# Kernel optimization log

Hardware: AMD Instinct MI355X
Metric: run time of the kernel (lower is better)

The kernel has to match this reference:

```python
import jax, jax.numpy as jnp
import numpy as np

B, S, H, NH = 4, 1024, 1024, 16
D = H // NH  # head dim = 64
MAXPOS = 1024
EPS = 1e-12


def setup_inputs() -> dict:
    key = jax.random.key(0)
    ks = jax.random.split(key, 12)
    sc = 0.02
    return {
        "hidden_states": jax.random.normal(ks[0], (B, S, H), jnp.float32),
        "attention_mask": jnp.zeros((B, 1, 1, S), jnp.float32),
        "Wq": jax.random.normal(ks[1], (H, H), jnp.float32) * sc,
        "bq": jnp.zeros((H,), jnp.float32),
        "Wk": jax.random.normal(ks[2], (H, H), jnp.float32) * sc,
        "bk": jnp.zeros((H,), jnp.float32),
        "Wv": jax.random.normal(ks[3], (H, H), jnp.float32) * sc,
        "bv": jnp.zeros((H,), jnp.float32),
        "dist_emb": jax.random.normal(ks[4], (2 * MAXPOS - 1, D), jnp.float32) * sc,
        "Wo": jax.random.normal(ks[5], (H, H), jnp.float32) * sc,
        "bo": jnp.zeros((H,), jnp.float32),
        "ln_g": jnp.ones((H,), jnp.float32),
        "ln_b": jnp.zeros((H,), jnp.float32),
    }


def _heads(x):  # [B,S,H] -> [B,NH,S,D]
    return x.reshape(B, S, NH, D).transpose(0, 2, 1, 3)


def reference(hidden_states, attention_mask, Wq, bq, Wk, bk, Wv, bv,
              dist_emb, Wo, bo, ln_g, ln_b):
    x = hidden_states
    q = _heads(x @ Wq.T + bq)  # [B,NH,S,D]
    k = _heads(x @ Wk.T + bk)
    v = _heads(x @ Wv.T + bv)

    scores = jnp.einsum("bhld,bhrd->bhlr", q, k)

    # relative_key_query positional bias
    pos = jnp.arange(S)
    distance = pos[:, None] - pos[None, :] + (MAXPOS - 1)  # [S,S]
    pe = dist_emb[distance]  # [S,S,D]
    scores = scores + jnp.einsum("bhld,lrd->bhlr", q, pe)
    scores = scores + jnp.einsum("bhrd,lrd->bhlr", k, pe)

    scores = scores / np.sqrt(D).astype(np.float32) + attention_mask
    probs = jax.nn.softmax(scores, axis=-1)  # dropout p=0 -> identity

    ctx = jnp.einsum("bhlr,bhrd->bhld", probs, v)
    ctx = ctx.transpose(0, 2, 1, 3).reshape(B, S, H)

    # BertSelfOutput: dense + residual + LayerNorm
    y = ctx @ Wo.T + bo + x
    mu = jnp.mean(y, axis=-1, keepdims=True)
    var = jnp.mean(jnp.square(y - mu), axis=-1, keepdims=True)
    return (y - mu) * jax.lax.rsqrt(var + EPS) * ln_g + ln_b
```

## Files before the change

### kernel.cpp

```cpp
#include <hip/hip_runtime.h>
#include <hip/hip_bf16.h>

#define BB 4
#define SS 1024
#define HH 1024
#define NHH 16
#define DD 64
#define MAXPOS 1024

typedef __hip_bfloat16 bf16;
typedef unsigned short ushort_t;
typedef __attribute__((ext_vector_type(8))) short short8;
typedef __attribute__((ext_vector_type(4))) float f32x4;
typedef __attribute__((ext_vector_type(4))) unsigned short us4;

#define MFMA_16x16x32(a, b, c) __builtin_amdgcn_mfma_f32_16x16x32_bf16((a), (b), (c), 0, 0, 0)

__device__ __forceinline__ float bu2f(ushort_t u) {
    union { unsigned int i; float f; } c; c.i = ((unsigned int)u) << 16; return c.f;
}
__device__ __forceinline__ ushort_t f2bu(float f) {
    __hip_bfloat16 h = __float2bfloat16(f);
    return *reinterpret_cast<ushort_t*>(&h);
}
__device__ __forceinline__ void stage16(const ushort_t* g, ushort_t* l) {
    __builtin_amdgcn_global_load_lds(
        (const __attribute__((address_space(1))) void*)g,
        (__attribute__((address_space(3))) void*)l,
        16, 0, 0);
}

__global__ void conv_all(const float* __restrict__ x,  const float* __restrict__ Wq,
                         const float* __restrict__ Wk, const float* __restrict__ Wv,
                         const float* __restrict__ Wo, const float* __restrict__ dist,
                         ushort_t* __restrict__ xb,  ushort_t* __restrict__ Wqb,
                         ushort_t* __restrict__ Wkb, ushort_t* __restrict__ Wvb,
                         ushort_t* __restrict__ Wob, ushort_t* __restrict__ Eb)
{
    const int i = blockIdx.x * 256 + threadIdx.x;
    const float* src; ushort_t* dst; int off;
    if (i < 1048576)      { src = x;  dst = xb;  off = i; }
    else if (i < 1310720) { src = Wq; dst = Wqb; off = i - 1048576; }
    else if (i < 1572864) { src = Wk; dst = Wkb; off = i - 1310720; }
    else if (i < 1835008) { src = Wv; dst = Wvb; off = i - 1572864; }
    else if (i < 2097152) { src = Wo; dst = Wob; off = i - 1835008; }
    else if (i < 2129920) {
        const int j = i - 2097152;
        float4 f = (j < 32752) ? ((const float4*)dist)[j] : make_float4(0.f, 0.f, 0.f, 0.f);
        us4 u;
        u[0] = f2bu(f.x); u[1] = f2bu(f.y); u[2] = f2bu(f.z); u[3] = f2bu(f.w);
        ((us4*)Eb)[j] = u;
        return;
    } else return;
    float4 f = ((const float4*)src)[off];
    us4 u;
    u[0] = f2bu(f.x); u[1] = f2bu(f.y); u[2] = f2bu(f.z); u[3] = f2bu(f.w);
    ((us4*)dst)[off] = u;
}

__global__ __launch_bounds__(256)
void qkv_mfma(const ushort_t* __restrict__ xb,
              const ushort_t* __restrict__ Wqb, const float* __restrict__ bq,
              const ushort_t* __restrict__ Wkb, const float* __restrict__ bk,
              const ushort_t* __restrict__ Wvb, const float* __restrict__ bv,
              ushort_t* __restrict__ q, ushort_t* __restrict__ k,
              ushort_t* __restrict__ vt)
{
    const int which = blockIdx.z;
    const ushort_t* __restrict__ W    = (which == 0) ? Wqb : (which == 1) ? Wkb : Wvb;
    const float*    __restrict__ bias = (which == 0) ? bq  : (which == 1) ? bk  : bv;

    const int tid = threadIdx.x, w = tid >> 6, lane = tid & 63;
    const int quad = lane >> 4, lq = lane & 15;
    const int wm = w >> 1, wn = w & 1;
    const int bm = blockIdx.y * 128;
    const int bn = blockIdx.x * 128;
    const int m0 = bm + wm * 64;
    const int n0 = bn + wn * 64;

    __shared__ __align__(16) ushort_t As[128 * 32];
    __shared__ __align__(16) ushort_t Bs[128 * 32];

    f32x4 acc[4][4];
#pragma unroll
    for (int i = 0; i < 4; i++)
#pragma unroll
        for (int j = 0; j < 4; j++) acc[i][j] = (f32x4){0.f, 0.f, 0.f, 0.f};

    const int lrow = lane >> 2;
    const int lcol = (lane & 3) * 8;
    const ushort_t* aS0 = xb + (size_t)(bm + w * 16 + lrow) * 1024 + lcol;
    const ushort_t* aS1 = aS0 + 64 * 1024;
    const ushort_t* bS0 = W  + (size_t)(bn + w * 16 + lrow) * 1024 + lcol;
    const ushort_t* bS1 = bS0 + 64 * 1024;
    ushort_t* const aD0 = As + w * 512;
    ushort_t* const aD1 = As + (w + 4) * 512;
    ushort_t* const bD0 = Bs + w * 512;
    ushort_t* const bD1 = Bs + (w + 4) * 512;

    for (int k0 = 0; k0 < 1024; k0 += 32) {
        __syncthreads();
        stage16(aS0 + k0, aD0);
        stage16(aS1 + k0, aD1);
        stage16(bS0 + k0, bD0);
        stage16(bS1 + k0, bD1);
        __syncthreads();

        short8 af[4], bf[4];
#pragma unroll
        for (int i = 0; i < 4; i++)
            af[i] = *(const short8*)&As[(wm * 64 + i * 16 + lq) * 32 + quad * 8];
#pragma unroll
        for (int j = 0; j < 4; j++)
            bf[j] = *(const short8*)&Bs[(wn * 64 + j * 16 + lq) * 32 + quad * 8];
#pragma unroll
        for (int i = 0; i < 4; i++)
#pragma unroll
            for (int j = 0; j < 4; j++)
                acc[i][j] = MFMA_16x16x32(af[i], bf[j], acc[i][j]);
    }

    if (which == 2) {
#pragma unroll
        for (int j = 0; j < 4; j++) {
            const int n  = n0 + j * 16 + lq;
            const int h_ = n >> 6, d_ = n & 63;
            const float bb = bias[n];
#pragma unroll
            for (int i = 0; i < 4; i++) {
                const int m  = m0 + i * 16 + quad * 4;
                const int b_ = m >> 10, l = m & 1023;
                us4 pv;
#pragma unroll
                for (int g = 0; g < 4; g++) pv[g] = f2bu(acc[i][j][g] + bb);
                *(us4*)(vt + (((size_t)(b_ * NHH) + h_) * DD + d_) * SS + l) = pv;
            }
        }
    } else {
        ushort_t* __restrict__ out = (which == 0) ? q : k;
        const float sc = (which == 0) ? 0.125f : 1.0f;
#pragma unroll
        for (int j = 0; j < 4; j++) {
            const int n  = n0 + j * 16 + lq;
            const int h_ = n >> 6, d_ = n & 63;
            const float bb = bias[n];
#pragma unroll
            for (int i = 0; i < 4; i++) {
#pragma unroll
                for (int g = 0; g < 4; g++) {
                    const int m  = m0 + i * 16 + quad * 4 + g;
                    const int b_ = m >> 10, l = m & 1023;
                    out[(((size_t)(b_ * NHH) + h_) * SS + l) * DD + d_] =
                        f2bu((acc[i][j][g] + bb) * sc);
                }
            }
        }
    }
}

__global__ __launch_bounds__(256)
void attn_mfma(const ushort_t* __restrict__ qb, const ushort_t* __restrict__ kb,
               const ushort_t* __restrict__ vt, const ushort_t* __restrict__ Eb,
               const float* __restrict__ mask, ushort_t* __restrict__ ctx)
{
    const int l0 = blockIdx.x * 64;
    const int h  = blockIdx.y, b = blockIdx.z;
    const int tid  = threadIdx.x;
    const int w    = tid >> 6;
    const int lane = tid & 63;
    const int quad = lane >> 4, lq = lane & 15;

    __shared__ __align__(16) ushort_t QEsT[128 * 68];
    __shared__ __align__(16) ushort_t KEsT[128 * 68];
    __shared__ __align__(16) ushort_t PsT [64 * 72];

    const ushort_t* qbh = qb + (size_t)(b * NHH + h) * SS * DD;
    const ushort_t* kbh = kb + (size_t)(b * NHH + h) * SS * DD;
    const ushort_t* vth = vt + (size_t)(b * NHH + h) * DD * SS;

    short8 qa0, qa1;
    {
        const ushort_t* p = qbh + (l0 + w * 16 + lq) * DD + quad * 8;
        qa0 = *(const short8*)p;
        qa1 = *(const short8*)(p + 32);
    }
    const int l_loc = w * 16 + lq;

    f32x4 Oacc[4];
#pragma unroll
    for (int dt = 0; dt < 4; dt++) Oacc[dt] = (f32x4){0.f, 0.f, 0.f, 0.f};
    float mrow = -3e38f, lrow = 0.f;

    for (int rt = 0; rt < 16; rt++) {
        const int r0   = rt * 64;
        const int dmin = l0 - r0 + 960;

        short8 kf0[4], kf1[4];
#pragma unroll
        for (int ct = 0; ct < 4; ct++) {
            const ushort_t* p = kbh + (r0 + ct * 16 + lq) * DD + quad * 8;
            kf0[ct] = *(const short8*)p;
            kf1[ct] = *(const short8*)(p + 32);
        }
        float mk[4];
#pragma unroll
        for (int g = 0; g < 4; g++) mk[g] = mask[b * SS + r0 + w * 16 + quad * 4 + g];

        __syncthreads();

#pragma unroll
        for (int tt = 0; tt < 8; tt++) {
            const ushort_t* ep = Eb + (size_t)(dmin + tt * 16 + lq) * DD + quad * 8;
            short8 e0 = *(const short8*)ep;
            short8 e1 = *(const short8*)(ep + 32);
            f32x4 qe = (f32x4){0.f, 0.f, 0.f, 0.f};
            f32x4 ke = (f32x4){0.f, 0.f, 0.f, 0.f};
            qe = MFMA_16x16x32(qa0, e0, qe);
            qe = MFMA_16x16x32(qa1, e1, qe);
            ke = MFMA_16x16x32(kf0[w], e0, ke);
            ke = MFMA_16x16x32(kf1[w], e1, ke);
            us4 pq, pk;
#pragma unroll
            for (int g = 0; g < 4; g++) {
                pq[g] = f2bu(qe[g]);
                pk[g] = f2bu(ke[g] * 0.125f + mk[g]);
            }
            const int trow = tt * 16 + lq;
            *(us4*)&QEsT[trow * 68 + w * 16 + quad * 4] = pq;
            *(us4*)&KEsT[trow * 68 + w * 16 + quad * 4] = pk;
        }

        f32x4 st[4];
#pragma unroll
        for (int ct = 0; ct < 4; ct++) {
            f32x4 a = (f32x4){0.f, 0.f, 0.f, 0.f};
            a = MFMA_16x16x32(kf0[ct], qa0, a);
            a = MFMA_16x16x32(kf1[ct], qa1, a);
            st[ct] = a;
        }

        __syncthreads();

        float p[4][4];
        float tmax = -3e38f;
#pragma unroll
        for (int ct = 0; ct < 4; ct++) {
#pragma unroll
            for (int g = 0; g < 4; g++) {
                const int r_loc = ct * 16 + quad * 4 + g;
                const int t = l_loc - r_loc + 63;
                float s = st[ct][g] + bu2f(QEsT[t * 68 + l_loc])
                                    + bu2f(KEsT[t * 68 + r_loc]);
                p[ct][g] = s;
                tmax = fmaxf(tmax, s);
            }
        }
        tmax = fmaxf(tmax, __shfl_xor(tmax, 16));
        tmax = fmaxf(tmax, __shfl_xor(tmax, 32));
        const float mnew  = fmaxf(mrow, tmax);
        const float alpha = __expf(mrow - mnew);
        mrow = mnew;
        float psum = 0.f;
#pragma unroll
        for (int ct = 0; ct < 4; ct++)
#pragma unroll
            for (int g = 0; g < 4; g++) {
                const float e = __expf(p[ct][g] - mrow);
                p[ct][g] = e;
                psum += e;
            }
        psum += __shfl_xor(psum, 16);
        psum += __shfl_xor(psum, 32);
        lrow = lrow * alpha + psum;
#pragma unroll
        for (int dt = 0; dt < 4; dt++)
#pragma unroll
            for (int g = 0; g < 4; g++) Oacc[dt][g] *= alpha;

#pragma unroll
        for (int ct = 0; ct < 4; ct++) {
            us4 pp;
#pragma unroll
            for (int g = 0; g < 4; g++) pp[g] = f2bu(p[ct][g]);
            *(us4*)&PsT[l_loc * 72 + ct * 16 + quad * 4] = pp;
        }

#pragma unroll
        for (int c = 0; c < 2; c++) {
            short8 pb = *(const short8*)&PsT[l_loc * 72 + c * 32 + quad * 8];
#pragma unroll
            for (int dt = 0; dt < 4; dt++) {
                const ushort_t* vp = vth + (size_t)(dt * 16 + lq) * SS
                                         + r0 + c * 32 + quad * 8;
                short8 va = *(const short8*)vp;
                Oacc[dt] = MFMA_16x16x32(va, pb, Oacc[dt]);
            }
        }
    }

    const float invl = 1.0f / lrow;
    ushort_t* cbase = ctx + (size_t)(b * SS + l0 + w * 16 + lq) * HH + h * DD;
#pragma unroll
    for (int dt = 0; dt < 4; dt++) {
        us4 po;
#pragma unroll
        for (int g = 0; g < 4; g++) po[g] = f2bu(Oacc[dt][g] * invl);
        *(us4*)(cbase + dt * 16 + quad * 4) = po;
    }
}

__global__ __launch_bounds__(256)
void out_proj(const ushort_t* __restrict__ ctx, const ushort_t* __restrict__ Wob,
              const float* __restrict__ bo, const float* __restrict__ x,
              float* __restrict__ y)
{
    const int tid = threadIdx.x, w = tid >> 6, lane = tid & 63;
    const int quad = lane >> 4, lq = lane & 15;
    const int wm = w >> 1, wn = w & 1;
    const int bm = blockIdx.y * 128;
    const int bn = blockIdx.x * 128;
    const int m0 = bm + wm * 64;
    const int n0 = bn + wn * 64;

    __shared__ __align__(16) ushort_t As[128 * 32];
    __shared__ __align__(16) ushort_t Bs[128 * 32];

    f32x4 acc[4][4];
#pragma unroll
    for (int i = 0; i < 4; i++)
#pragma unroll
        for (int j = 0; j < 4; j++) acc[i][j] = (f32x4){0.f, 0.f, 0.f, 0.f};

    const int lrow = lane >> 2;
    const int lcol = (lane & 3) * 8;
    const ushort_t* aS0 = ctx + (size_t)(bm + w * 16 + lrow) * 1024 + lcol;
    const ushort_t* aS1 = aS0 + 64 * 1024;
    const ushort_t* bS0 = Wob + (size_t)(bn + w * 16 + lrow) * 1024 + lcol;
    const ushort_t* bS1 = bS0 + 64 * 1024;
    ushort_t* const aD0 = As + w * 512;
    ushort_t* const aD1 = As + (w + 4) * 512;
    ushort_t* const bD0 = Bs + w * 512;
    ushort_t* const bD1 = Bs + (w + 4) * 512;

    for (int k0 = 0; k0 < 1024; k0 += 32) {
        __syncthreads();
        stage16(aS0 + k0, aD0);
        stage16(aS1 + k0, aD1);
        stage16(bS0 + k0, bD0);
        stage16(bS1 + k0, bD1);
        __syncthreads();

        short8 af[4], bf[4];
#pragma unroll
        for (int i = 0; i < 4; i++)
            af[i] = *(const short8*)&As[(wm * 64 + i * 16 + lq) * 32 + quad * 8];
#pragma unroll
        for (int j = 0; j < 4; j++)
            bf[j] = *(const short8*)&Bs[(wn * 64 + j * 16 + lq) * 32 + quad * 8];
#pragma unroll
        for (int i = 0; i < 4; i++)
#pragma unroll
            for (int j = 0; j < 4; j++)
                acc[i][j] = MFMA_16x16x32(af[i], bf[j], acc[i][j]);
    }

#pragma unroll
    for (int j = 0; j < 4; j++) {
        const int n = n0 + j * 16 + lq;
        const float bb = bo[n];
#pragma unroll
        for (int i = 0; i < 4; i++) {
#pragma unroll
            for (int g = 0; g < 4; g++) {
                const int m = m0 + i * 16 + quad * 4 + g;
                y[(size_t)m * 1024 + n] = acc[i][j][g] + bb + x[(size_t)m * 1024 + n];
            }
        }
    }
}

__global__ void layernorm(const float* __restrict__ y, const float* __restrict__ g,
                          const float* __restrict__ beta, float* __restrict__ out)
{
    const int row = blockIdx.x;
    const int tid = threadIdx.x;

    __shared__ float red[256];
    __shared__ float red2[256];

    const float4 t4 = *(const float4*)(y + (size_t)row * 1024 + tid * 4);
    float s  = t4.x + t4.y + t4.z + t4.w;
    float s2 = t4.x * t4.x + t4.y * t4.y + t4.z * t4.z + t4.w * t4.w;
    red[tid] = s;
    red2[tid] = s2;
    __syncthreads();
    for (int st = 128; st > 0; st >>= 1) {
        if (tid < st) { red[tid] += red[tid + st]; red2[tid] += red2[tid + st]; }
        __syncthreads();
    }
    const float mu  = red[0] * (1.0f / 1024.0f);
    const float var = red2[0] * (1.0f / 1024.0f) - mu * mu;
    const float rs  = rsqrtf(var + 1e-12f);

    const float4 g4 = *(const float4*)(g + tid * 4);
    const float4 b4 = *(const float4*)(beta + tid * 4);
    float4 o;
    o.x = (t4.x - mu) * rs * g4.x + b4.x;
    o.y = (t4.y - mu) * rs * g4.y + b4.y;
    o.z = (t4.z - mu) * rs * g4.z + b4.z;
    o.w = (t4.w - mu) * rs * g4.w + b4.w;
    *(float4*)(out + (size_t)row * 1024 + tid * 4) = o;
}

extern "C" void kernel_launch(void* const* d_in, const int* in_sizes, int n_in,
                              void* d_out, int out_size, void* d_ws, size_t ws_size,
                              hipStream_t stream)
{
    const float* x    = (const float*)d_in[0];
    const float* mask = (const float*)d_in[1];
    const float* Wq   = (const float*)d_in[2];
    const float* bq   = (const float*)d_in[3];
    const float* Wk   = (const float*)d_in[4];
    const float* bk   = (const float*)d_in[5];
    const float* Wv   = (const float*)d_in[6];
    const float* bv   = (const float*)d_in[7];
    const float* dist = (const float*)d_in[8];
    const float* Wo   = (const float*)d_in[9];
    const float* bo   = (const float*)d_in[10];
    const float* g    = (const float*)d_in[11];
    const float* be   = (const float*)d_in[12];

    char* wsb = (char*)d_ws;
    ushort_t* xb  = (ushort_t*)(wsb);
    ushort_t* Wqb = (ushort_t*)(wsb + ( 8u << 20));
    ushort_t* Wkb = (ushort_t*)(wsb + (10u << 20));
    ushort_t* Wvb = (ushort_t*)(wsb + (12u << 20));
    ushort_t* Wob = (ushort_t*)(wsb + (14u << 20));
    ushort_t* qbu = (ushort_t*)(wsb + (16u << 20));
    ushort_t* kbu = (ushort_t*)(wsb + (24u << 20));
    ushort_t* vtb = (ushort_t*)(wsb + (32u << 20));
    ushort_t* Eb  = (ushort_t*)(wsb + (40u << 20));
    float*    y   = (float*)(wsb + (16u << 20));
    ushort_t* ctxb = (ushort_t*)d_out;

    conv_all<<<8320, 256, 0, stream>>>(x, Wq, Wk, Wv, Wo, dist,
                                       xb, Wqb, Wkb, Wvb, Wob, Eb);
    qkv_mfma<<<dim3(8, 32, 3), 256, 0, stream>>>(xb, Wqb, bq, Wkb, bk, Wvb, bv,
                                                 qbu, kbu, vtb);
    attn_mfma<<<dim3(16, 16, 4), 256, 0, stream>>>(qbu, kbu, vtb, Eb, mask, ctxb);
    out_proj<<<dim3(8, 32), 256, 0, stream>>>(ctxb, Wob, bo, x, y);
    layernorm<<<4096, 256, 0, stream>>>(y, g, be, (float*)d_out);
}
```

Measured before the change: 414.3 us.

## Swap MFMA operands for vectorized epilogue stores and batch two attention jobs per block

Splits the fused QKV projection into a Q/K kernel and a separate V kernel. The Q/K and output projections now swap the MFMA operand order so each lane holds four consecutive columns, which lets the epilogue use 8-byte bf16 stores and float4 loads and stores for bias, residual and output instead of scalar accesses. The attention kernel launches 512 blocks that each run two (query tile, head, batch) jobs in sequence, halving the grid at some cost in parallelism. The result is an extra kernel launch and fewer resident attention blocks in exchange for coalesced epilogue memory traffic.

```diff
diff --git a/kernel.cpp b/kernel.cpp
--- a/kernel.cpp
+++ b/kernel.cpp
@@ -59,16 +59,16 @@
 }
 
 __global__ __launch_bounds__(256)
-void qkv_mfma(const ushort_t* __restrict__ xb,
-              const ushort_t* __restrict__ Wqb, const float* __restrict__ bq,
-              const ushort_t* __restrict__ Wkb, const float* __restrict__ bk,
-              const ushort_t* __restrict__ Wvb, const float* __restrict__ bv,
-              ushort_t* __restrict__ q, ushort_t* __restrict__ k,
-              ushort_t* __restrict__ vt)
+void qk_mfma(const ushort_t* __restrict__ xb,
+             const ushort_t* __restrict__ Wqb, const float* __restrict__ bq,
+             const ushort_t* __restrict__ Wkb, const float* __restrict__ bk,
+             ushort_t* __restrict__ q, ushort_t* __restrict__ k)
 {
     const int which = blockIdx.z;
-    const ushort_t* __restrict__ W    = (which == 0) ? Wqb : (which == 1) ? Wkb : Wvb;
-    const float*    __restrict__ bias = (which == 0) ? bq  : (which == 1) ? bk  : bv;
+    const ushort_t* __restrict__ W    = which ? Wkb : Wqb;
+    const float*    __restrict__ bias = which ? bk  : bq;
+    ushort_t*       __restrict__ out  = which ? k   : q;
+    const float sc = which ? 1.0f : 0.125f;
 
     const int tid = threadIdx.x, w = tid >> 6, lane = tid & 63;
     const int quad = lane >> 4, lq = lane & 15;
@@ -117,43 +117,96 @@
         for (int i = 0; i < 4; i++)
 #pragma unroll
             for (int j = 0; j < 4; j++)
+                acc[i][j] = MFMA_16x16x32(bf[j], af[i], acc[i][j]);
+    }
+
+#pragma unroll
+    for (int j = 0; j < 4; j++) {
+        const int nb = n0 + j * 16 + quad * 4;
+        const int h_ = nb >> 6, db = nb & 63;
+        const float4 b4 = *(const float4*)&bias[nb];
+#pragma unroll
+        for (int i = 0; i < 4; i++) {
+            const int m  = m0 + i * 16 + lq;
+            const int b_ = m >> 10, l = m & 1023;
+            us4 pv;
+            pv[0] = f2bu((acc[i][j][0] + b4.x) * sc);
+            pv[1] = f2bu((acc[i][j][1] + b4.y) * sc);
+            pv[2] = f2bu((acc[i][j][2] + b4.z) * sc);
+            pv[3] = f2bu((acc[i][j][3] + b4.w) * sc);
+            *(us4*)(out + (((size_t)(b_ * NHH) + h_) * SS + l) * DD + db) = pv;
+        }
+    }
+}
+
+__global__ __launch_bounds__(256)
+void v_mfma(const ushort_t* __restrict__ xb,
+            const ushort_t* __restrict__ Wvb, const float* __restrict__ bv,
+            ushort_t* __restrict__ vt)
+{
+    const int tid = threadIdx.x, w = tid >> 6, lane = tid & 63;
+    const int quad = lane >> 4, lq = lane & 15;
+    const int wm = w >> 1, wn = w & 1;
+    const int bm = blockIdx.y * 128;
+    const int bn = blockIdx.x * 128;
+    const int m0 = bm + wm * 64;
+    const int n0 = bn + wn * 64;
+
+    __shared__ __align__(16) ushort_t As[128 * 32];
+    __shared__ __align__(16) ushort_t Bs[128 * 32];
+
+    f32x4 acc[4][4];
+#pragma unroll
+    for (int i = 0; i < 4; i++)
+#pragma unroll
+        for (int j = 0; j < 4; j++) acc[i][j] = (f32x4){0.f, 0.f, 0.f, 0.f};
+
+    const int lrow = lane >> 2;
+    const int lcol = (lane & 3) * 8;
+    const ushort_t* aS0 = xb  + (size_t)(bm + w * 16 + lrow) * 1024 + lcol;
+    const ushort_t* aS1 = aS0 + 64 * 1024;
+    const ushort_t* bS0 = Wvb + (size_t)(bn + w * 16 + lrow) * 1024 + lcol;
+    const ushort_t* bS1 = bS0 + 64 * 1024;
+    ushort_t* const aD0 = As + w * 512;
+    ushort_t* const aD1 = As + (w + 4) * 512;
+    ushort_t* const bD0 = Bs + w * 512;
+    ushort_t* const bD1 = Bs + (w + 4) * 512;
+
+    for (int k0 = 0; k0 < 1024; k0 += 32) {
+        __syncthreads();
+        stage16(aS0 + k0, aD0);
+        stage16(aS1 + k0, aD1);
+        stage16(bS0 + k0, bD0);
+        stage16(bS1 + k0, bD1);
+        __syncthreads();
+
+        short8 af[4], bf[4];
+#pragma unroll
+        for (int i = 0; i < 4; i++)
+            af[i] = *(const short8*)&As[(wm * 64 + i * 16 + lq) * 32 + quad * 8];
+#pragma unroll
+        for (int j = 0; j < 4; j++)
+            bf[j] = *(const short8*)&Bs[(wn * 64 + j * 16 + lq) * 32 + quad * 8];
+#pragma unroll
+        for (int i = 0; i < 4; i++)
+#pragma unroll
+            for (int j = 0; j < 4; j++)
                 acc[i][j] = MFMA_16x16x32(af[i], bf[j], acc[i][j]);
     }
 
-    if (which == 2) {
-#pragma unroll
-        for (int j = 0; j < 4; j++) {
-            const int n  = n0 + j * 16 + lq;
-            const int h_ = n >> 6, d_ = n & 63;
-            const float bb = bias[n];
-#pragma unroll
-            for (int i = 0; i < 4; i++) {
-                const int m  = m0 + i * 16 + quad * 4;
-                const int b_ = m >> 10, l = m & 1023;
-                us4 pv;
-#pragma unroll
-                for (int g = 0; g < 4; g++) pv[g] = f2bu(acc[i][j][g] + bb);
-                *(us4*)(vt + (((size_t)(b_ * NHH) + h_) * DD + d_) * SS + l) = pv;
-            }
-        }
-    } else {
-        ushort_t* __restrict__ out = (which == 0) ? q : k;
-        const float sc = (which == 0) ? 0.125f : 1.0f;
-#pragma unroll
-        for (int j = 0; j < 4; j++) {
-            const int n  = n0 + j * 16 + lq;
-            const int h_ = n >> 6, d_ = n & 63;
-            const float bb = bias[n];
-#pragma unroll
-            for (int i = 0; i < 4; i++) {
-#pragma unroll
-                for (int g = 0; g < 4; g++) {
-                    const int m  = m0 + i * 16 + quad * 4 + g;
-                    const int b_ = m >> 10, l = m & 1023;
-                    out[(((size_t)(b_ * NHH) + h_) * SS + l) * DD + d_] =
-                        f2bu((acc[i][j][g] + bb) * sc);
-                }
-            }
+#pragma unroll
+    for (int j = 0; j < 4; j++) {
+        const int n  = n0 + j * 16 + lq;
+        const int h_ = n >> 6, d_ = n & 63;
+        const float bb = bv[n];
+#pragma unroll
+        for (int i = 0; i < 4; i++) {
+            const int m  = m0 + i * 16 + quad * 4;
+            const int b_ = m >> 10, l = m & 1023;
+            us4 pv;
+#pragma unroll
+            for (int g = 0; g < 4; g++) pv[g] = f2bu(acc[i][j][g] + bb);
+            *(us4*)(vt + (((size_t)(b_ * NHH) + h_) * DD + d_) * SS + l) = pv;
         }
     }
 }
@@ -163,8 +216,6 @@
                const ushort_t* __restrict__ vt, const ushort_t* __restrict__ Eb,
                const float* __restrict__ mask, ushort_t* __restrict__ ctx)
 {
-    const int l0 = blockIdx.x * 64;
-    const int h  = blockIdx.y, b = blockIdx.z;
     const int tid  = threadIdx.x;
     const int w    = tid >> 6;
     const int lane = tid & 63;
@@ -174,138 +225,145 @@
     __shared__ __align__(16) ushort_t KEsT[128 * 68];
     __shared__ __align__(16) ushort_t PsT [64 * 72];
 
-    const ushort_t* qbh = qb + (size_t)(b * NHH + h) * SS * DD;
-    const ushort_t* kbh = kb + (size_t)(b * NHH + h) * SS * DD;
-    const ushort_t* vth = vt + (size_t)(b * NHH + h) * DD * SS;
-
-    short8 qa0, qa1;
-    {
-        const ushort_t* p = qbh + (l0 + w * 16 + lq) * DD + quad * 8;
-        qa0 = *(const short8*)p;
-        qa1 = *(const short8*)(p + 32);
-    }
-    const int l_loc = w * 16 + lq;
-
-    f32x4 Oacc[4];
-#pragma unroll
-    for (int dt = 0; dt < 4; dt++) Oacc[dt] = (f32x4){0.f, 0.f, 0.f, 0.f};
-    float mrow = -3e38f, lrow = 0.f;
-
-    for (int rt = 0; rt < 16; rt++) {
-        const int r0   = rt * 64;
-        const int dmin = l0 - r0 + 960;
-
-        short8 kf0[4], kf1[4];
-#pragma unroll
-        for (int ct = 0; ct < 4; ct++) {
-            const ushort_t* p = kbh + (r0 + ct * 16 + lq) * DD + quad * 8;
-            kf0[ct] = *(const short8*)p;
-            kf1[ct] = *(const short8*)(p + 32);
+    for (int jj = 0; jj < 2; jj++) {
+        const int job = blockIdx.x * 2 + jj;
+        const int l0  = (job & 15) * 64;
+        const int h   = (job >> 4) & 15;
+        const int b   = job >> 8;
+
+        const ushort_t* qbh = qb + (size_t)(b * NHH + h) * SS * DD;
+        const ushort_t* kbh = kb + (size_t)(b * NHH + h) * SS * DD;
+        const ushort_t* vth = vt + (size_t)(b * NHH + h) * DD * SS;
+
+        short8 qa0, qa1;
+        {
+            const ushort_t* p = qbh + (l0 + w * 16 + lq) * DD + quad * 8;
+            qa0 = *(const short8*)p;
+            qa1 = *(const short8*)(p + 32);
         }
-        float mk[4];
-#pragma unroll
-        for (int g = 0; g < 4; g++) mk[g] = mask[b * SS + r0 + w * 16 + quad * 4 + g];
-
-        __syncthreads();
-
-#pragma unroll
-        for (int tt = 0; tt < 8; tt++) {
-            const ushort_t* ep = Eb + (size_t)(dmin + tt * 16 + lq) * DD + quad * 8;
-            short8 e0 = *(const short8*)ep;
-            short8 e1 = *(const short8*)(ep + 32);
-            f32x4 qe = (f32x4){0.f, 0.f, 0.f, 0.f};
-            f32x4 ke = (f32x4){0.f, 0.f, 0.f, 0.f};
-            qe = MFMA_16x16x32(qa0, e0, qe);
-            qe = MFMA_16x16x32(qa1, e1, qe);
-            ke = MFMA_16x16x32(kf0[w], e0, ke);
-            ke = MFMA_16x16x32(kf1[w], e1, ke);
-            us4 pq, pk;
-#pragma unroll
-            for (int g = 0; g < 4; g++) {
-                pq[g] = f2bu(qe[g]);
-                pk[g] = f2bu(ke[g] * 0.125f + mk[g]);
+        const int l_loc = w * 16 + lq;
+
+        f32x4 Oacc[4];
+#pragma unroll
+        for (int dt = 0; dt < 4; dt++) Oacc[dt] = (f32x4){0.f, 0.f, 0.f, 0.f};
+        float mrow = -3e38f, lrow = 0.f;
+
+        for (int rt = 0; rt < 16; rt++) {
+            const int r0   = rt * 64;
+            const int dmin = l0 - r0 + 960;
+
+            short8 kf0[4], kf1[4];
+#pragma unroll
+            for (int ct = 0; ct < 4; ct++) {
+                const ushort_t* p = kbh + (r0 + ct * 16 + lq) * DD + quad * 8;
+                kf0[ct] = *(const short8*)p;
+                kf1[ct] = *(const short8*)(p + 32);
             }
-            const int trow = tt * 16 + lq;
-            *(us4*)&QEsT[trow * 68 + w * 16 + quad * 4] = pq;
-            *(us4*)&KEsT[trow * 68 + w * 16 + quad * 4] = pk;
-        }
-
-        f32x4 st[4];
-#pragma unroll
-        for (int ct = 0; ct < 4; ct++) {
-            f32x4 a = (f32x4){0.f, 0.f, 0.f, 0.f};
-            a = MFMA_16x16x32(kf0[ct], qa0, a);
-            a = MFMA_16x16x32(kf1[ct], qa1, a);
-            st[ct] = a;
-        }
-
-        __syncthreads();
-
-        float p[4][4];
-        float tmax = -3e38f;
-#pragma unroll
-        for (int ct = 0; ct < 4; ct++) {
-#pragma unroll
-            for (int g = 0; g < 4; g++) {
-                const int r_loc = ct * 16 + quad * 4 + g;
-                const int t = l_loc - r_loc + 63;
-                float s = st[ct][g] + bu2f(QEsT[t * 68 + l_loc])
-                                    + bu2f(KEsT[t * 68 + r_loc]);
-                p[ct][g] = s;
-                tmax = fmaxf(tmax, s);
+            float mk[4];
+#pragma unroll
+            for (int g = 0; g < 4; g++) mk[g] = mask[b * SS + r0 + w * 16 + quad * 4 + g];
+
+            __syncthreads();
+
+#pragma unroll
+            for (int tt = 0; tt < 8; tt++) {
+                const ushort_t* ep = Eb + (size_t)(dmin + tt * 16 + lq) * DD + quad * 8;
+                short8 e0 = *(const short8*)ep;
+                short8 e1 = *(const short8*)(ep + 32);
+                f32x4 qe = (f32x4){0.f, 0.f, 0.f, 0.f};
+                f32x4 ke = (f32x4){0.f, 0.f, 0.f, 0.f};
+                qe = MFMA_16x16x32(qa0, e0, qe);
+                qe = MFMA_16x16x32(qa1, e1, qe);
+                ke = MFMA_16x16x32(kf0[w], e0, ke);
+                ke = MFMA_16x16x32(kf1[w], e1, ke);
+                us4 pq, pk;
+#pragma unroll
+                for (int g = 0; g < 4; g++) {
+                    pq[g] = f2bu(qe[g]);
+                    pk[g] = f2bu(ke[g] * 0.125f + mk[g]);
+                }
+                const int trow = tt * 16 + lq;
+                *(us4*)&QEsT[trow * 68 + w * 16 + quad * 4] = pq;
+                *(us4*)&KEsT[trow * 68 + w * 16 + quad * 4] = pk;
+            }
+
+            f32x4 st[4];
+#pragma unroll
+            for (int ct = 0; ct < 4; ct++) {
+                f32x4 a = (f32x4){0.f, 0.f, 0.f, 0.f};
+                a = MFMA_16x16x32(kf0[ct], qa0, a);
+                a = MFMA_16x16x32(kf1[ct], qa1, a);
+                st[ct] = a;
+            }
+
+            __syncthreads();
+
+            float p[4][4];
+            float tmax = -3e38f;
+#pragma unroll
+            for (int ct = 0; ct < 4; ct++) {
+#pragma unroll
+                for (int g = 0; g < 4; g++) {
+                    const int r_loc = ct * 16 + quad * 4 + g;
+                    const int t = l_loc - r_loc + 63;
+                    float s = st[ct][g] + bu2f(QEsT[t * 68 + l_loc])
+                                        + bu2f(KEsT[t * 68 + r_loc]);
+                    p[ct][g] = s;
+                    tmax = fmaxf(tmax, s);
+                }
+            }
+            tmax = fmaxf(tmax, __shfl_xor(tmax, 16));
+            tmax = fmaxf(tmax, __shfl_xor(tmax, 32));
+            const float mnew  = fmaxf(mrow, tmax);
+            const float alpha = __expf(mrow - mnew);
+            mrow = mnew;
+            float psum = 0.f;
+#pragma unroll
+            for (int ct = 0; ct < 4; ct++)
+#pragma unroll
+                for (int g = 0; g < 4; g++) {
+                    const float e = __expf(p[ct][g] - mrow);
+                    p[ct][g] = e;
+                    psum += e;
+                }
+            psum += __shfl_xor(psum, 16);
+            psum += __shfl_xor(psum, 32);
+            lrow = lrow * alpha + psum;
+#pragma unroll
+            for (int dt = 0; dt < 4; dt++)
+#pragma unroll
+                for (int g = 0; g < 4; g++) Oacc[dt][g] *= alpha;
+
+#pragma unroll
+            for (int ct = 0; ct < 4; ct++) {
+                us4 pp;
+#pragma unroll
+                for (int g = 0; g < 4; g++) pp[g] = f2bu(p[ct][g]);
+                *(us4*)&PsT[l_loc * 72 + ct * 16 + quad * 4] = pp;
+            }
+
+#pragma unroll
+            for (int c = 0; c < 2; c++) {
+                short8 pb = *(const short8*)&PsT[l_loc * 72 + c * 32 + quad * 8];
+#pragma unroll
+                for (int dt = 0; dt < 4; dt++) {
+                    const ushort_t* vp = vth + (size_t)(dt * 16 + lq) * SS
+                                             + r0 + c * 32 + quad * 8;
+                    short8 va = *(const short8*)vp;
+                    Oacc[dt] = MFMA_16x16x32(va, pb, Oacc[dt]);
+                }
             }
         }
-        tmax = fmaxf(tmax, __shfl_xor(tmax, 16));
-        tmax = fmaxf(tmax, __shfl_xor(tmax, 32));
-        const float mnew  = fmaxf(mrow, tmax);
-        const float alpha = __expf(mrow - mnew);
-        mrow = mnew;
-        float psum = 0.f;
-#pragma unroll
-        for (int ct = 0; ct < 4; ct++)
-#pragma unroll
-            for (int g = 0; g < 4; g++) {
-                const float e = __expf(p[ct][g] - mrow);
-                p[ct][g] = e;
-                psum += e;
-            }
-        psum += __shfl_xor(psum, 16);
-        psum += __shfl_xor(psum, 32);
-        lrow = lrow * alpha + psum;
-#pragma unroll
-        for (int dt = 0; dt < 4; dt++)
-#pragma unroll
-            for (int g = 0; g < 4; g++) Oacc[dt][g] *= alpha;
-
-#pragma unroll
-        for (int ct = 0; ct < 4; ct++) {
-            us4 pp;
-#pragma unroll
-            for (int g = 0; g < 4; g++) pp[g] = f2bu(p[ct][g]);
-            *(us4*)&PsT[l_loc * 72 + ct * 16 + quad * 4] = pp;
+
+        const float invl = 1.0f / lrow;
+        ushort_t* cbase = ctx + (size_t)(b * SS + l0 + w * 16 + lq) * HH + h * DD;
+#pragma unroll
+        for (int dt = 0; dt < 4; dt++) {
+            us4 po;
+#pragma unroll
+            for (int g = 0; g < 4; g++) po[g] = f2bu(Oacc[dt][g] * invl);
+            *(us4*)(cbase + dt * 16 + quad * 4) = po;
         }
-
-#pragma unroll
-        for (int c = 0; c < 2; c++) {
-            short8 pb = *(const short8*)&PsT[l_loc * 72 + c * 32 + quad * 8];
-#pragma unroll
-            for (int dt = 0; dt < 4; dt++) {
-                const ushort_t* vp = vth + (size_t)(dt * 16 + lq) * SS
-                                         + r0 + c * 32 + quad * 8;
-                short8 va = *(const short8*)vp;
-                Oacc[dt] = MFMA_16x16x32(va, pb, Oacc[dt]);
-            }
-        }
-    }
-
-    const float invl = 1.0f / lrow;
-    ushort_t* cbase = ctx + (size_t)(b * SS + l0 + w * 16 + lq) * HH + h * DD;
-#pragma unroll
-    for (int dt = 0; dt < 4; dt++) {
-        us4 po;
-#pragma unroll
-        for (int g = 0; g < 4; g++) po[g] = f2bu(Oacc[dt][g] * invl);
-        *(us4*)(cbase + dt * 16 + quad * 4) = po;
     }
 }
 
@@ -361,20 +419,23 @@
         for (int i = 0; i < 4; i++)
 #pragma unroll
             for (int j = 0; j < 4; j++)
-                acc[i][j] = MFMA_16x16x32(af[i], bf[j], acc[i][j]);
+                acc[i][j] = MFMA_16x16x32(bf[j], af[i], acc[i][j]);
     }
 
 #pragma unroll
     for (int j = 0; j < 4; j++) {
-        const int n = n0 + j * 16 + lq;
-        const float bb = bo[n];
+        const int nb = n0 + j * 16 + quad * 4;
+        const float4 b4 = *(const float4*)&bo[nb];
 #pragma unroll
         for (int i = 0; i < 4; i++) {
-#pragma unroll
-            for (int g = 0; g < 4; g++) {
-                const int m = m0 + i * 16 + quad * 4 + g;
-                y[(size_t)m * 1024 + n] = acc[i][j][g] + bb + x[(size_t)m * 1024 + n];
-            }
+            const int m = m0 + i * 16 + lq;
+            const float4 xr = *(const float4*)&x[(size_t)m * 1024 + nb];
+            float4 o;
+            o.x = acc[i][j][0] + b4.x + xr.x;
+            o.y = acc[i][j][1] + b4.y + xr.y;
+            o.z = acc[i][j][2] + b4.z + xr.z;
+            o.w = acc[i][j][3] + b4.w + xr.w;
+            *(float4*)&y[(size_t)m * 1024 + nb] = o;
         }
     }
 }
@@ -445,9 +506,9 @@
 
     conv_all<<<8320, 256, 0, stream>>>(x, Wq, Wk, Wv, Wo, dist,
                                        xb, Wqb, Wkb, Wvb, Wob, Eb);
-    qkv_mfma<<<dim3(8, 32, 3), 256, 0, stream>>>(xb, Wqb, bq, Wkb, bk, Wvb, bv,
-                                                 qbu, kbu, vtb);
-    attn_mfma<<<dim3(16, 16, 4), 256, 0, stream>>>(qbu, kbu, vtb, Eb, mask, ctxb);
+    qk_mfma<<<dim3(8, 32, 2), 256, 0, stream>>>(xb, Wqb, bq, Wkb, bk, qbu, kbu);
+    v_mfma<<<dim3(8, 32), 256, 0, stream>>>(xb, Wvb, bv, vtb);
+    attn_mfma<<<512, 256, 0, stream>>>(qbu, kbu, vtb, Eb, mask, ctxb);
     out_proj<<<dim3(8, 32), 256, 0, stream>>>(ctxb, Wob, bo, x, y);
     layernorm<<<4096, 256, 0, stream>>>(y, g, be, (float*)d_out);
 }
```

Result: slower. 589.2 us (+42.2%).
